# Kernel optimization log

Measured on AMD Instinct MI355X. Metric: run time of the kernel, lower is better.

The kernel has to match this reference:

```python
import jax, jax.numpy as jnp
import numpy as np

H, C = 2, 32  # heads, out_channels per head
NEG_SLOPE = 0.2


def gatv2_layer(h, src, dst, ea, W, b, We, att, bias, N):
    # shared lin_l = lin_r (share_weights=True)
    z = (h @ W + b).reshape(N, H, C)                      # [N,H,C]
    e = (ea @ We).reshape(-1, H, C)                        # [E',H,C]
    s = jax.nn.leaky_relu(z[dst] + z[src] + e, NEG_SLOPE)  # [E',H,C]
    alpha = jnp.einsum('ehc,hc->eh', s, att)               # [E',H]
    # segment softmax over destination neighborhoods
    m = jax.ops.segment_max(alpha, dst, num_segments=N)
    m = jnp.where(jnp.isfinite(m), m, 0.0)
    ex = jnp.exp(alpha - m[dst])
    denom = jax.ops.segment_sum(ex, dst, num_segments=N)
    a = ex / (denom[dst] + 1e-16)                          # [E',H]
    msg = (z[src] * a[:, :, None]).reshape(-1, H * C)      # [E',H*C]
    out = jax.ops.segment_sum(msg, dst, num_segments=N) + bias
    return out                                             # [N,H*C]


def setup_inputs() -> dict:
    key = jax.random.key(0)
    ks = jax.random.split(key, 16)
    N, E = 50000, 800000
    inp = {
        'x': jax.random.normal(ks[0], (N, 2), jnp.float32),
        'edge_index': jax.random.randint(ks[1], (2, E), 0, N, jnp.int64 if jax.config.jax_enable_x64 else jnp.int32).astype(jnp.int32),
        'edge_attr': jax.random.uniform(ks[2], (E, 2), jnp.float32),
        'dest_index': 123,
        'W0': jax.random.normal(ks[3], (2, 64), jnp.float32) * 0.5,
        'b0': jnp.zeros((64,), jnp.float32),
        'We0': jax.random.normal(ks[4], (2, 64), jnp.float32) * 0.5,
        'att0': jax.random.normal(ks[5], (H, C), jnp.float32) * 0.5,
        'bias0': jnp.zeros((64,), jnp.float32),
        'W1': jax.random.normal(ks[6], (64, 64), jnp.float32) * 0.125,
        'b1': jnp.zeros((64,), jnp.float32),
        'We1': jax.random.normal(ks[7], (2, 64), jnp.float32) * 0.5,
        'att1': jax.random.normal(ks[8], (H, C), jnp.float32) * 0.5,
        'bias1': jnp.zeros((64,), jnp.float32),
        'Wm1': jax.random.normal(ks[9], (194, 32), jnp.float32) * 0.07,
        'bm1': jnp.zeros((32,), jnp.float32),
        'Wm2': jax.random.normal(ks[10], (32, 1), jnp.float32) * 0.17,
        'bm2': jnp.zeros((1,), jnp.float32),
    }
    return inp


def reference(x, edge_index, edge_attr, dest_index,
              W0, b0, We0, att0, bias0,
              W1, b1, We1, att1, bias1,
              Wm1, bm1, Wm2, bm2):
    N = x.shape[0]
    # add self loops (fill_value='mean' for edge_attr)
    loops = jnp.arange(N, dtype=edge_index.dtype)
    src = jnp.concatenate([edge_index[0], loops])
    dst = jnp.concatenate([edge_index[1], loops])
    ea_sl = jnp.concatenate(
        [edge_attr, jnp.broadcast_to(edge_attr.mean(axis=0), (N, edge_attr.shape[1]))], axis=0)

    h = x
    h = jax.nn.elu(gatv2_layer(h, src, dst, ea_sl, W0, b0, We0, att0, bias0, N))
    h = jax.nn.elu(gatv2_layer(h, src, dst, ea_sl, W1, b1, We1, att1, bias1, N))

    goal = h[dest_index]                                   # [64]
    src_emb = h[edge_index[0]]                             # [E,64]
    dst_emb = h[edge_index[1]]                             # [E,64]
    goal_rep = jnp.broadcast_to(goal, (edge_index.shape[1], goal.shape[0]))
    edge_in = jnp.concatenate([src_emb, dst_emb, goal_rep, edge_attr], axis=-1)  # [E,194]
    hmlp = jax.nn.relu(edge_in @ Wm1 + bm1)
    logits = (hmlp @ Wm2 + bm2).squeeze(-1)                # [E]
    return logits
```

## Files before the change

kernel.cpp:

```cpp
#include <hip/hip_runtime.h>
#include <hip/hip_bf16.h>
#include <hip/hip_fp16.h>
#include <math.h>


typedef __attribute__((ext_vector_type(8))) short short8;
typedef __attribute__((ext_vector_type(4))) float f32x4;

#define BSH 6
#define CAP 2048
#define CH 4096

template <int IMM>
__device__ __forceinline__ float swz(float x) {
    return __int_as_float(__builtin_amdgcn_ds_swizzle(__float_as_int(x), IMM));
}

template <int CTRL>
__device__ __forceinline__ float dpp_add(float p) {
    int t = __builtin_amdgcn_update_dpp(0, __float_as_int(p), CTRL, 0xF, 0xF, true);
    return p + __int_as_float(t);
}

__device__ __forceinline__ short2 bsplit(float x) {
    unsigned u = __float_as_uint(x);
    short hi = (short)(u >> 16);
    float hif = __uint_as_float(u & 0xFFFF0000u);
    short lo = (short)(__float_as_uint(x - hif) >> 16);
    return make_short2(hi, lo);
}

__global__ __launch_bounds__(512) void setup_kernel(const float* __restrict__ W1,
                                                    const float* __restrict__ Wm1,
                                                    short* __restrict__ BfW1,
                                                    short* __restrict__ BfWm,
                                                    int* __restrict__ bucket_cursor,
                                                    float* __restrict__ easum, int nbuck) {
    if (blockIdx.x == 2) {
        for (int i = threadIdx.x; i < nbuck; i += 512) bucket_cursor[i] = i * CAP;
        if (threadIdx.x < 2) easum[threadIdx.x] = 0.f;
        return;
    }
    int snt = threadIdx.x >> 6;
    int lane = threadIdx.x & 63;
    int s = snt >> 2, nt = snt & 3;
    int col = nt * 16 + (lane & 15);
    short* Bf = blockIdx.x == 0 ? BfW1 : BfWm;
#pragma unroll
    for (int j = 0; j < 8; ++j) {
        int k = s * 32 + (lane >> 4) * 8 + j;
        float v;
        if (blockIdx.x == 0) {
            v = W1[k * 64 + col];
        } else {
            v = (col < 32) ? Wm1[k * 32 + col] : Wm1[(64 + k) * 32 + (col - 32)];
        }
        short2 t = bsplit(v);
        Bf[(snt * 2 + 0) * 512 + lane * 8 + j] = t.x;
        Bf[(snt * 2 + 1) * 512 + lane * 8 + j] = t.y;
    }
}

__global__ __launch_bounds__(256) void phaseA_kernel(const int* __restrict__ ei,
                                                     const float2* __restrict__ ea,
                                                     int* __restrict__ bucket_cursor,
                                                     float* __restrict__ easum,
                                                     float4* __restrict__ staged,
                                                     int E, int nbuck) {
    extern __shared__ int sm[];
    int* lcnt = sm;
    int* lbase = sm + nbuck;
    __shared__ float r0[4], r1[4];
    int tid = threadIdx.x;
    for (int i = tid; i < nbuck; i += 256) lcnt[i] = 0;
    __syncthreads();
    int base = blockIdx.x * CH;
    int end = min(base + CH, E);
    for (int i = base + tid; i < end; i += 256) {
        int d = ei[E + i];
        atomicAdd(&lcnt[d >> BSH], 1);
    }
    __syncthreads();
    for (int i = tid; i < nbuck; i += 256) {
        int c = lcnt[i];
        lbase[i] = c ? atomicAdd(&bucket_cursor[i], c) : 0;
        lcnt[i] = 0;
    }
    __syncthreads();
    float s0 = 0.f, s1 = 0.f;
    for (int i = base + tid; i < end; i += 256) {
        int s = ei[i], d = ei[E + i];
        float2 v = ea[i];
        s0 += v.x; s1 += v.y;
        int b = d >> BSH;
        int pos = lbase[b] + atomicAdd(&lcnt[b], 1);
        staged[pos] = make_float4(__int_as_float(s), v.x, v.y, __int_as_float(d));
    }
#pragma unroll
    for (int o = 32; o >= 1; o >>= 1) {
        s0 += __shfl_xor(s0, o);
        s1 += __shfl_xor(s1, o);
    }
    int wave = tid >> 6;
    if ((tid & 63) == 0) { r0[wave] = s0; r1[wave] = s1; }
    __syncthreads();
    if (tid == 0) {
        atomicAdd(&easum[0], r0[0] + r0[1] + r0[2] + r0[3]);
        atomicAdd(&easum[1], r1[0] + r1[1] + r1[2] + r1[3]);
    }
}

__global__ __launch_bounds__(512) void phaseB_mega(
    const float4* __restrict__ staged, const int* __restrict__ bucket_cursor,
    const float* __restrict__ easum, const float2* __restrict__ x,
    const float* __restrict__ W0, const float* __restrict__ b0,
    const float* __restrict__ We, const float* __restrict__ att,
    const float* __restrict__ bias, const short* __restrict__ Bf,
    const float* __restrict__ b1,
    int* __restrict__ row_ptr, float4* __restrict__ recs,
    __half* __restrict__ z16, int N, int E, int nbuck) {
    __shared__ int cnt64[64];
    __shared__ int offs[64];
    __shared__ int psum[512];
    __shared__ float acc6[64][6];
    __shared__ float h0s[64 * 64];
    int b = blockIdx.x;
    int n0g = b << BSH;
    int tid = threadIdx.x;
    int local = 0;
    for (int j = tid; j < b; j += 512) local += bucket_cursor[j] - j * CAP;
    psum[tid] = local;
    if (tid < 64) cnt64[tid] = 0;
    for (int i = tid; i < 64 * 6; i += 512) ((float*)acc6)[i] = 0.f;
    __syncthreads();
    for (int st = 256; st > 0; st >>= 1) {
        if (tid < st) psum[tid] += psum[tid + st];
        __syncthreads();
    }
    int bbase = psum[0] + 64 * b;
    int sbeg = b * CAP;
    int send = bucket_cursor[b];
    for (int i = sbeg + tid; i < send; i += 512) {
        int d = __float_as_int(staged[i].w);
        atomicAdd(&cnt64[d - n0g], 1);
    }
    __syncthreads();
    int node = n0g + tid;
    int tot = 0;
    if (tid < 64) {
        tot = cnt64[tid] + ((node < N) ? 1 : 0);
        offs[tid] = tot;
    }
    __syncthreads();
    for (int st = 1; st < 64; st <<= 1) {
        int v = 0;
        if (tid < 64) {
            v = offs[tid];
            if (tid >= st) v += offs[tid - st];
        }
        __syncthreads();
        if (tid < 64) offs[tid] = v;
        __syncthreads();
    }
    float invE = 1.f / (float)E;
    float m0 = easum[0] * invE, m1 = easum[1] * invE;
    if (tid < 64 && node < N) {
        int excl = bbase + offs[tid] - tot;
        row_ptr[node] = excl;
        recs[excl] = make_float4(__int_as_float(node), m0, m1, __int_as_float(node));
        offs[tid] = excl + 1;
    }
    int nodes_here = min(64, N - n0g);
    int nrec = (send - sbeg) + nodes_here;
    if (b == nbuck - 1 && tid == 0) row_ptr[N] = bbase + nrec;
    __syncthreads();
    for (int i = sbeg + tid; i < send; i += 512) {
        float4 r = staged[i];
        int d = __float_as_int(r.w);
        int pos = atomicAdd(&offs[d - n0g], 1);
        recs[pos] = r;
    }
    __syncthreads();

    int lane = tid & 63;
    int m = lane & 15, quad = lane >> 4;
    int wave = tid >> 6;
    {
        int c0 = quad * 8, c1 = 32 + c0;
        float w0a[8], w1a[8], ata[8], w0b[8], w1b[8], atb[8];
        float Wxa[8], Wya[8], bca[8], Wxb[8], Wyb[8], bcb[8];
#pragma unroll
        for (int j = 0; j < 8; ++j) {
            w0a[j] = We[c0 + j];  w1a[j] = We[64 + c0 + j];  ata[j] = att[c0 + j];
            w0b[j] = We[c1 + j];  w1b[j] = We[64 + c1 + j];  atb[j] = att[c1 + j];
            Wxa[j] = W0[c0 + j];  Wya[j] = W0[64 + c0 + j];  bca[j] = b0[c0 + j];
            Wxb[j] = W0[c1 + j];  Wyb[j] = W0[64 + c1 + j];  bcb[j] = b0[c1 + j];
        }
        int ntile = (nrec + 15) >> 4;
        for (int t = wave; t < ntile; t += 8) {
            int el = m * ntile + t;
            bool valid = el < nrec;
            int e = bbase + (valid ? el : nrec - 1);
            float4 r = recs[e];
            int s = __float_as_int(r.x);
            int d = __float_as_int(r.w);
            float2 xs = x[s];
            float2 xd = x[d];
            float P0 = 0.f, P1 = 0.f;
#pragma unroll
            for (int j = 0; j < 8; ++j) {
                float zs = fmaf(xs.x, Wxa[j], fmaf(xs.y, Wya[j], bca[j]));
                float zd = fmaf(xd.x, Wxa[j], fmaf(xd.y, Wya[j], bca[j]));
                float t0 = zd + zs + fmaf(r.y, w0a[j], r.z * w1a[j]);
                t0 = fmaxf(t0, 0.2f * t0);
                P0 = fmaf(t0, ata[j], P0);
                float zs1 = fmaf(xs.x, Wxb[j], fmaf(xs.y, Wyb[j], bcb[j]));
                float zd1 = fmaf(xd.x, Wxb[j], fmaf(xd.y, Wyb[j], bcb[j]));
                float t1 = zd1 + zs1 + fmaf(r.y, w0b[j], r.z * w1b[j]);
                t1 = fmaxf(t1, 0.2f * t1);
                P1 = fmaf(t1, atb[j], P1);
            }
            P0 += swz<0x401F>(P0);
            P1 += swz<0x401F>(P1);
            P0 += __shfl_xor(P0, 32);
            P1 += __shfl_xor(P1, 32);
            float w0 = __expf(fminf(P0, 60.f));
            float w1 = __expf(fminf(P1, 60.f));
            if (lane < 16 && valid) {
                int dl = d - n0g;
                atomicAdd(&acc6[dl][0], w0);
                atomicAdd(&acc6[dl][1], w0 * xs.x);
                atomicAdd(&acc6[dl][2], w0 * xs.y);
                atomicAdd(&acc6[dl][3], w1);
                atomicAdd(&acc6[dl][4], w1 * xs.x);
                atomicAdd(&acc6[dl][5], w1 * xs.y);
            }
        }
    }
    __syncthreads();

    for (int idx = tid; idx < nodes_here * 64; idx += 512) {
        int q = idx >> 6;
        int ch = idx & 63;
        int hsel = (ch >= 32) ? 3 : 0;
        float l  = acc6[q][hsel];
        float Sx = acc6[q][hsel + 1];
        float Sy = acc6[q][hsel + 2];
        float num = fmaf(W0[ch], Sx, fmaf(W0[64 + ch], Sy, b0[ch] * l));
        float v = num / (l + 1e-16f) + bias[ch];
        v = (v > 0.f) ? v : expm1f(v);
        h0s[idx] = v;
    }
    for (int idx = nodes_here * 64 + tid; idx < 64 * 64; idx += 512) h0s[idx] = 0.f;
    __syncthreads();

    int rowb = (wave & 3) * 16 + m;
    int ntb = (wave >> 2) * 2;
    f32x4 acc[2] = {{0.f, 0.f, 0.f, 0.f}, {0.f, 0.f, 0.f, 0.f}};
#pragma unroll
    for (int s = 0; s < 2; ++s) {
        const float* ap = h0s + rowb * 64 + s * 32 + quad * 8;
        float4 a0 = *(const float4*)ap;
        float4 a1 = *(const float4*)(ap + 4);
        short8 ahi, alo;
        short2 t;
        t = bsplit(a0.x); ahi[0] = t.x; alo[0] = t.y;
        t = bsplit(a0.y); ahi[1] = t.x; alo[1] = t.y;
        t = bsplit(a0.z); ahi[2] = t.x; alo[2] = t.y;
        t = bsplit(a0.w); ahi[3] = t.x; alo[3] = t.y;
        t = bsplit(a1.x); ahi[4] = t.x; alo[4] = t.y;
        t = bsplit(a1.y); ahi[5] = t.x; alo[5] = t.y;
        t = bsplit(a1.z); ahi[6] = t.x; alo[6] = t.y;
        t = bsplit(a1.w); ahi[7] = t.x; alo[7] = t.y;
#pragma unroll
        for (int u = 0; u < 2; ++u) {
            const short* bp = Bf + ((s * 4 + ntb + u) * 2) * 512 + lane * 8;
            short8 bhi = *(const short8*)bp;
            short8 blo = *(const short8*)(bp + 512);
            acc[u] = __builtin_amdgcn_mfma_f32_16x16x32_bf16(ahi, bhi, acc[u], 0, 0, 0);
            acc[u] = __builtin_amdgcn_mfma_f32_16x16x32_bf16(ahi, blo, acc[u], 0, 0, 0);
            acc[u] = __builtin_amdgcn_mfma_f32_16x16x32_bf16(alo, bhi, acc[u], 0, 0, 0);
        }
    }
#pragma unroll
    for (int u = 0; u < 2; ++u) {
        int col = (ntb + u) * 16 + m;
        float bj = b1[col];
#pragma unroll
        for (int r = 0; r < 4; ++r) {
            int orow = n0g + (wave & 3) * 16 + quad * 4 + r;
            if (orow < N) z16[(size_t)orow * 64 + col] = __float2half(acc[u][r] + bj);
        }
    }
}

__global__ __launch_bounds__(256) void agg1_kernel(
    const __half* __restrict__ z, const int* __restrict__ row_ptr,
    const float4* __restrict__ recs,
    const float* __restrict__ We, const float* __restrict__ att,
    const float* __restrict__ bias, float* __restrict__ hout, int N) {
    int gtid = blockIdx.x * blockDim.x + threadIdx.x;
    int n = gtid >> 6;
    if (n >= N) return;
    n = __builtin_amdgcn_readfirstlane(n);
    int lane = threadIdx.x & 63;
    int half = lane >> 5;
    int c = (lane & 31) * 2;

    float We0a = We[c],      We0b = We[c + 1];
    float We1a = We[64 + c], We1b = We[64 + c + 1];
    float atta = att[c],     attb = att[c + 1];
    float2 znf = __half22float2(*(const __half2*)(z + (size_t)n * 64 + c));

    int beg = row_ptr[n], end = row_ptr[n + 1];
    float ll[4] = {0.f, 0.f, 0.f, 0.f};
    float a0[4] = {0.f, 0.f, 0.f, 0.f};
    float a1[4] = {0.f, 0.f, 0.f, 0.f};
    for (int i = beg; i < end; i += 8) {
        float w[4]; float2 zs[4];
#pragma unroll
        for (int k = 0; k < 4; ++k) {
            int idx = i + 2 * k + half;
            int idc = idx < end ? idx : end - 1;
            float4 r = recs[idc];
            int s = __float_as_int(r.x);
            zs[k] = __half22float2(*(const __half2*)(z + (size_t)s * 64 + c));
            float sj0 = znf.x + zs[k].x + fmaf(r.y, We0a, r.z * We1a);
            float sj1 = znf.y + zs[k].y + fmaf(r.y, We0b, r.z * We1b);
            sj0 = fmaxf(sj0, 0.2f * sj0);
            sj1 = fmaxf(sj1, 0.2f * sj1);
            float p = fmaf(sj0, atta, sj1 * attb);
            p = dpp_add<0xB1>(p);
            p = dpp_add<0x4E>(p);
            p = dpp_add<0x141>(p);
            p = dpp_add<0x140>(p);
            float ww = __expf(fminf(p, 60.f));
            w[k] = (idx < end) ? ww : 0.f;
        }
#pragma unroll
        for (int k = 0; k < 4; ++k) {
            ll[k] += w[k];
            a0[k] = fmaf(w[k], zs[k].x, a0[k]);
            a1[k] = fmaf(w[k], zs[k].y, a1[k]);
        }
    }
    float l  = (ll[0] + ll[1]) + (ll[2] + ll[3]);
    float s0 = (a0[0] + a0[1]) + (a0[2] + a0[3]);
    float s1 = (a1[0] + a1[1]) + (a1[2] + a1[3]);
    l  += __shfl_xor(l, 32);
    s0 += __shfl_xor(s0, 32);
    s1 += __shfl_xor(s1, 32);
    float inv = 1.f / (l + 1e-16f);
    float v0 = s0 * inv + bias[c];
    float v1 = s1 * inv + bias[c + 1];
    v0 = (v0 > 0.f) ? v0 : expm1f(v0);
    v1 = (v1 > 0.f) ? v1 : expm1f(v1);
    *(float2*)(hout + (size_t)n * 64 + c) = make_float2(v0, v1);
}

__global__ __launch_bounds__(256) void mfma_gemm64(const float* __restrict__ h,
                                                   const short* __restrict__ Bf,
                                                   __half* __restrict__ out, int N,
                                                   const float* __restrict__ Wm1,
                                                   const float* __restrict__ bm1,
                                                   const int* __restrict__ dest,
                                                   float* __restrict__ gv) {
    int wave = threadIdx.x >> 6;
    int lane = threadIdx.x & 63;
    int n0 = blockIdx.x * 64 + wave * 16;
    if (n0 < N) {
        int m = lane & 15, quad = lane >> 4;
        int arow = n0 + m;
        if (arow > N - 1) arow = N - 1;
        f32x4 acc[4] = {{0.f, 0.f, 0.f, 0.f}, {0.f, 0.f, 0.f, 0.f},
                        {0.f, 0.f, 0.f, 0.f}, {0.f, 0.f, 0.f, 0.f}};
#pragma unroll
        for (int s = 0; s < 2; ++s) {
            const float* ap = h + (size_t)arow * 64 + s * 32 + quad * 8;
            float4 a0 = *(const float4*)ap;
            float4 a1 = *(const float4*)(ap + 4);
            short8 ahi, alo;
            short2 t;
            t = bsplit(a0.x); ahi[0] = t.x; alo[0] = t.y;
            t = bsplit(a0.y); ahi[1] = t.x; alo[1] = t.y;
            t = bsplit(a0.z); ahi[2] = t.x; alo[2] = t.y;
            t = bsplit(a0.w); ahi[3] = t.x; alo[3] = t.y;
            t = bsplit(a1.x); ahi[4] = t.x; alo[4] = t.y;
            t = bsplit(a1.y); ahi[5] = t.x; alo[5] = t.y;
            t = bsplit(a1.z); ahi[6] = t.x; alo[6] = t.y;
            t = bsplit(a1.w); ahi[7] = t.x; alo[7] = t.y;
#pragma unroll
            for (int nt = 0; nt < 4; ++nt) {
                const short* bp = Bf + ((s * 4 + nt) * 2) * 512 + lane * 8;
                short8 bhi = *(const short8*)bp;
                short8 blo = *(const short8*)(bp + 512);
                acc[nt] = __builtin_amdgcn_mfma_f32_16x16x32_bf16(ahi, bhi, acc[nt], 0, 0, 0);
                acc[nt] = __builtin_amdgcn_mfma_f32_16x16x32_bf16(ahi, blo, acc[nt], 0, 0, 0);
                acc[nt] = __builtin_amdgcn_mfma_f32_16x16x32_bf16(alo, bhi, acc[nt], 0, 0, 0);
            }
        }
#pragma unroll
        for (int nt = 0; nt < 4; ++nt) {
            int col = nt * 16 + m;
#pragma unroll
            for (int r = 0; r < 4; ++r) {
                int orow = n0 + quad * 4 + r;
                if (orow < N) out[(size_t)orow * 64 + col] = __float2half(acc[nt][r]);
            }
        }
    }
    if (gv && blockIdx.x == 0 && threadIdx.x < 32) {
        int dd = dest[0];
        int q = threadIdx.x;
        float acc2 = bm1[q];
        for (int k = 0; k < 64; ++k)
            acc2 = fmaf(h[(size_t)dd * 64 + k], Wm1[(128 + k) * 32 + q], acc2);
        gv[q] = acc2;
    }
}

__global__ __launch_bounds__(256) void edge_mlp_kernel(
    const int* __restrict__ ei, const float2* __restrict__ ea,
    const __half* __restrict__ hsd, const float* __restrict__ gvec,
    const float* __restrict__ WrowA, const float* __restrict__ WrowB,
    const float* __restrict__ Wm2, const float* __restrict__ bm2,
    float* __restrict__ out, int E) {
    int tid = blockIdx.x * blockDim.x + threadIdx.x;
    int e = tid >> 3;
    int j = tid & 7;
    if (e >= E) return;
    int s = ei[e], d = ei[E + e];
    float2 eav = ea[e];
    const __half2* ps = (const __half2*)(hsd + (size_t)s * 64 + j * 4);
    const __half2* pd = (const __half2*)(hsd + (size_t)d * 64 + 32 + j * 4);
    float2 a01 = __half22float2(ps[0]), a23 = __half22float2(ps[1]);
    float2 b01 = __half22float2(pd[0]), b23 = __half22float2(pd[1]);
    float4 g = *(const float4*)(gvec + j * 4);
    float4 wa = *(const float4*)(WrowA + j * 4);
    float4 wb = *(const float4*)(WrowB + j * 4);
    float4 w2 = *(const float4*)(Wm2 + j * 4);
    float acc = 0.f, v;
    v = fmaf(eav.x, wa.x, fmaf(eav.y, wb.x, a01.x + b01.x + g.x)); v = fmaxf(v, 0.f); acc = fmaf(v, w2.x, acc);
    v = fmaf(eav.x, wa.y, fmaf(eav.y, wb.y, a01.y + b01.y + g.y)); v = fmaxf(v, 0.f); acc = fmaf(v, w2.y, acc);
    v = fmaf(eav.x, wa.z, fmaf(eav.y, wb.z, a23.x + b23.x + g.z)); v = fmaxf(v, 0.f); acc = fmaf(v, w2.z, acc);
    v = fmaf(eav.x, wa.w, fmaf(eav.y, wb.w, a23.y + b23.y + g.w)); v = fmaxf(v, 0.f); acc = fmaf(v, w2.w, acc);
    acc = dpp_add<0xB1>(acc);
    acc = dpp_add<0x4E>(acc);
    acc = dpp_add<0x141>(acc);
    if (j == 0) out[e] = acc + bm2[0];
}

extern "C" void kernel_launch(void* const* d_in, const int* in_sizes, int n_in,
                              void* d_out, int out_size, void* d_ws, size_t ws_size,
                              hipStream_t stream) {
    const float* x     = (const float*)d_in[0];
    const int*   ei    = (const int*)d_in[1];
    const float* ea    = (const float*)d_in[2];
    const int*   dest  = (const int*)d_in[3];
    const float* W0    = (const float*)d_in[4];
    const float* b0    = (const float*)d_in[5];
    const float* We0   = (const float*)d_in[6];
    const float* att0  = (const float*)d_in[7];
    const float* bias0 = (const float*)d_in[8];
    const float* W1    = (const float*)d_in[9];
    const float* b1    = (const float*)d_in[10];
    const float* We1   = (const float*)d_in[11];
    const float* att1  = (const float*)d_in[12];
    const float* bias1 = (const float*)d_in[13];
    const float* Wm1   = (const float*)d_in[14];
    const float* bm1   = (const float*)d_in[15];
    const float* Wm2   = (const float*)d_in[16];
    const float* bm2   = (const float*)d_in[17];

    const int N = in_sizes[0] / 2;
    const int E = in_sizes[1] / 2;
    const int nbuck = (N + 63) >> BSH;
    const int nchunk = (E + CH - 1) / CH;

    char* ws = (char*)d_ws;
    size_t off = 0;
    auto alloc = [&](size_t bytes) -> void* {
        void* p = ws + off;
        off += bytes;
        off = (off + 255) & ~(size_t)255;
        return p;
    };
    int*    bucket_cursor = (int*)alloc((size_t)nbuck * 4);
    int*    row_ptr       = (int*)alloc((size_t)(N + 1) * 4);
    size_t  slack_bytes   = (size_t)nbuck * CAP * 16;
    float4* staged        = (float4*)alloc(slack_bytes);
    float4* recs          = (float4*)alloc((size_t)(E + N) * 16);
    __half* z16           = (__half*)alloc((size_t)N * 64 * 2);
    float*  hbuf          = (float*)alloc((size_t)N * 64 * 4);
    float*  easum         = (float*)alloc(8);
    float*  gvec          = (float*)alloc(32 * 4);
    short*  BfW1          = (short*)alloc(8192 * 2);
    short*  BfWm          = (short*)alloc(8192 * 2);
    __half* hsd16         = z16;

    dim3 blk(256);
    setup_kernel<<<3, 512, 0, stream>>>(W1, Wm1, BfW1, BfWm, bucket_cursor, easum, nbuck);
    phaseA_kernel<<<nchunk, blk, (size_t)nbuck * 8, stream>>>(ei, (const float2*)ea,
                                                              bucket_cursor, easum,
                                                              staged, E, nbuck);
    phaseB_mega<<<nbuck, 512, 0, stream>>>(staged, bucket_cursor, easum,
                                           (const float2*)x, W0, b0, We0, att0, bias0,
                                           BfW1, b1, row_ptr, recs, z16, N, E, nbuck);
    agg1_kernel<<<(N * 64 + 255) / 256, blk, 0, stream>>>(z16, row_ptr, recs,
                                                          We1, att1, bias1, hbuf, N);
    mfma_gemm64<<<(N + 63) / 64, blk, 0, stream>>>(hbuf, BfWm, hsd16, N,
                                                   Wm1, bm1, dest, gvec);
    edge_mlp_kernel<<<((size_t)E * 8 + 255) / 256, blk, 0, stream>>>(
        ei, (const float2*)ea, hsd16, gvec,
        Wm1 + 192 * 32, Wm1 + 193 * 32, Wm2, bm2, (float*)d_out, E);
}
```

Measured before the change: 256.9 us.

## Fuse layer-2 aggregation with MLP projection GEMM and shrink phaseB blocks

Merges the per-node layer-2 attention aggregation and the following MFMA projection GEMM into one kernel. Each 256-thread block aggregates 64 nodes into LDS and multiplies them by the packed MLP weights there, so the fp32 hidden buffer no longer makes a round trip through global memory and one launch is removed. The goal-vector dot product now reads from LDS in whichever block owns the dest node. phaseB_mega also drops from 512 to 256 threads, so each wave now covers all four output tiles of its 16 rows. The trade-off is fewer waves per block for latency hiding, and a serial 16-node loop per wave in the fused kernel.

```diff
diff --git a/kernel.cpp b/kernel.cpp
--- a/kernel.cpp
+++ b/kernel.cpp
@@ -110,7 +110,7 @@
     }
 }
 
-__global__ __launch_bounds__(512) void phaseB_mega(
+__global__ __launch_bounds__(256) void phaseB_mega(
     const float4* __restrict__ staged, const int* __restrict__ bucket_cursor,
     const float* __restrict__ easum, const float2* __restrict__ x,
     const float* __restrict__ W0, const float* __restrict__ b0,
@@ -121,26 +121,26 @@
     __half* __restrict__ z16, int N, int E, int nbuck) {
     __shared__ int cnt64[64];
     __shared__ int offs[64];
-    __shared__ int psum[512];
+    __shared__ int psum[256];
     __shared__ float acc6[64][6];
     __shared__ float h0s[64 * 64];
     int b = blockIdx.x;
     int n0g = b << BSH;
     int tid = threadIdx.x;
     int local = 0;
-    for (int j = tid; j < b; j += 512) local += bucket_cursor[j] - j * CAP;
+    for (int j = tid; j < b; j += 256) local += bucket_cursor[j] - j * CAP;
     psum[tid] = local;
     if (tid < 64) cnt64[tid] = 0;
-    for (int i = tid; i < 64 * 6; i += 512) ((float*)acc6)[i] = 0.f;
-    __syncthreads();
-    for (int st = 256; st > 0; st >>= 1) {
+    for (int i = tid; i < 64 * 6; i += 256) ((float*)acc6)[i] = 0.f;
+    __syncthreads();
+    for (int st = 128; st > 0; st >>= 1) {
         if (tid < st) psum[tid] += psum[tid + st];
         __syncthreads();
     }
     int bbase = psum[0] + 64 * b;
     int sbeg = b * CAP;
     int send = bucket_cursor[b];
-    for (int i = sbeg + tid; i < send; i += 512) {
+    for (int i = sbeg + tid; i < send; i += 256) {
         int d = __float_as_int(staged[i].w);
         atomicAdd(&cnt64[d - n0g], 1);
     }
@@ -174,7 +174,7 @@
     int nrec = (send - sbeg) + nodes_here;
     if (b == nbuck - 1 && tid == 0) row_ptr[N] = bbase + nrec;
     __syncthreads();
-    for (int i = sbeg + tid; i < send; i += 512) {
+    for (int i = sbeg + tid; i < send; i += 256) {
         float4 r = staged[i];
         int d = __float_as_int(r.w);
         int pos = atomicAdd(&offs[d - n0g], 1);
@@ -197,7 +197,7 @@
             Wxb[j] = W0[c1 + j];  Wyb[j] = W0[64 + c1 + j];  bcb[j] = b0[c1 + j];
         }
         int ntile = (nrec + 15) >> 4;
-        for (int t = wave; t < ntile; t += 8) {
+        for (int t = wave; t < ntile; t += 4) {
             int el = m * ntile + t;
             bool valid = el < nrec;
             int e = bbase + (valid ? el : nrec - 1);
@@ -239,7 +239,7 @@
     }
     __syncthreads();
 
-    for (int idx = tid; idx < nodes_here * 64; idx += 512) {
+    for (int idx = tid; idx < nodes_here * 64; idx += 256) {
         int q = idx >> 6;
         int ch = idx & 63;
         int hsel = (ch >= 32) ? 3 : 0;
@@ -251,12 +251,12 @@
         v = (v > 0.f) ? v : expm1f(v);
         h0s[idx] = v;
     }
-    for (int idx = nodes_here * 64 + tid; idx < 64 * 64; idx += 512) h0s[idx] = 0.f;
-    __syncthreads();
-
-    int rowb = (wave & 3) * 16 + m;
-    int ntb = (wave >> 2) * 2;
-    f32x4 acc[2] = {{0.f, 0.f, 0.f, 0.f}, {0.f, 0.f, 0.f, 0.f}};
+    for (int idx = nodes_here * 64 + tid; idx < 64 * 64; idx += 256) h0s[idx] = 0.f;
+    __syncthreads();
+
+    int rowb = wave * 16 + m;
+    f32x4 acc[4] = {{0.f, 0.f, 0.f, 0.f}, {0.f, 0.f, 0.f, 0.f},
+                    {0.f, 0.f, 0.f, 0.f}, {0.f, 0.f, 0.f, 0.f}};
 #pragma unroll
     for (int s = 0; s < 2; ++s) {
         const float* ap = h0s + rowb * 64 + s * 32 + quad * 8;
@@ -273,149 +273,152 @@
         t = bsplit(a1.z); ahi[6] = t.x; alo[6] = t.y;
         t = bsplit(a1.w); ahi[7] = t.x; alo[7] = t.y;
 #pragma unroll
-        for (int u = 0; u < 2; ++u) {
-            const short* bp = Bf + ((s * 4 + ntb + u) * 2) * 512 + lane * 8;
+        for (int nt = 0; nt < 4; ++nt) {
+            const short* bp = Bf + ((s * 4 + nt) * 2) * 512 + lane * 8;
             short8 bhi = *(const short8*)bp;
             short8 blo = *(const short8*)(bp + 512);
-            acc[u] = __builtin_amdgcn_mfma_f32_16x16x32_bf16(ahi, bhi, acc[u], 0, 0, 0);
-            acc[u] = __builtin_amdgcn_mfma_f32_16x16x32_bf16(ahi, blo, acc[u], 0, 0, 0);
-            acc[u] = __builtin_amdgcn_mfma_f32_16x16x32_bf16(alo, bhi, acc[u], 0, 0, 0);
-        }
-    }
-#pragma unroll
-    for (int u = 0; u < 2; ++u) {
-        int col = (ntb + u) * 16 + m;
+            acc[nt] = __builtin_amdgcn_mfma_f32_16x16x32_bf16(ahi, bhi, acc[nt], 0, 0, 0);
+            acc[nt] = __builtin_amdgcn_mfma_f32_16x16x32_bf16(ahi, blo, acc[nt], 0, 0, 0);
+            acc[nt] = __builtin_amdgcn_mfma_f32_16x16x32_bf16(alo, bhi, acc[nt], 0, 0, 0);
+        }
+    }
+#pragma unroll
+    for (int nt = 0; nt < 4; ++nt) {
+        int col = nt * 16 + m;
         float bj = b1[col];
 #pragma unroll
         for (int r = 0; r < 4; ++r) {
-            int orow = n0g + (wave & 3) * 16 + quad * 4 + r;
-            if (orow < N) z16[(size_t)orow * 64 + col] = __float2half(acc[u][r] + bj);
-        }
-    }
-}
-
-__global__ __launch_bounds__(256) void agg1_kernel(
+            int orow = n0g + wave * 16 + quad * 4 + r;
+            if (orow < N) z16[(size_t)orow * 64 + col] = __float2half(acc[nt][r] + bj);
+        }
+    }
+}
+
+__global__ __launch_bounds__(256) void agg1_gemm_kernel(
     const __half* __restrict__ z, const int* __restrict__ row_ptr,
     const float4* __restrict__ recs,
     const float* __restrict__ We, const float* __restrict__ att,
-    const float* __restrict__ bias, float* __restrict__ hout, int N) {
-    int gtid = blockIdx.x * blockDim.x + threadIdx.x;
-    int n = gtid >> 6;
-    if (n >= N) return;
-    n = __builtin_amdgcn_readfirstlane(n);
-    int lane = threadIdx.x & 63;
+    const float* __restrict__ bias, const short* __restrict__ Bf,
+    __half* __restrict__ out, int N,
+    const float* __restrict__ Wm1, const float* __restrict__ bm1,
+    const int* __restrict__ dest, float* __restrict__ gv) {
+    __shared__ float hlds[64 * 64];
+    int tid = threadIdx.x;
+    int wave = tid >> 6;
+    int lane = tid & 63;
     int half = lane >> 5;
     int c = (lane & 31) * 2;
+    int n0 = blockIdx.x * 64;
 
     float We0a = We[c],      We0b = We[c + 1];
     float We1a = We[64 + c], We1b = We[64 + c + 1];
     float atta = att[c],     attb = att[c + 1];
-    float2 znf = __half22float2(*(const __half2*)(z + (size_t)n * 64 + c));
-
-    int beg = row_ptr[n], end = row_ptr[n + 1];
-    float ll[4] = {0.f, 0.f, 0.f, 0.f};
-    float a0[4] = {0.f, 0.f, 0.f, 0.f};
-    float a1[4] = {0.f, 0.f, 0.f, 0.f};
-    for (int i = beg; i < end; i += 8) {
-        float w[4]; float2 zs[4];
-#pragma unroll
-        for (int k = 0; k < 4; ++k) {
-            int idx = i + 2 * k + half;
-            int idc = idx < end ? idx : end - 1;
-            float4 r = recs[idc];
-            int s = __float_as_int(r.x);
-            zs[k] = __half22float2(*(const __half2*)(z + (size_t)s * 64 + c));
-            float sj0 = znf.x + zs[k].x + fmaf(r.y, We0a, r.z * We1a);
-            float sj1 = znf.y + zs[k].y + fmaf(r.y, We0b, r.z * We1b);
-            sj0 = fmaxf(sj0, 0.2f * sj0);
-            sj1 = fmaxf(sj1, 0.2f * sj1);
-            float p = fmaf(sj0, atta, sj1 * attb);
-            p = dpp_add<0xB1>(p);
-            p = dpp_add<0x4E>(p);
-            p = dpp_add<0x141>(p);
-            p = dpp_add<0x140>(p);
-            float ww = __expf(fminf(p, 60.f));
-            w[k] = (idx < end) ? ww : 0.f;
-        }
-#pragma unroll
-        for (int k = 0; k < 4; ++k) {
-            ll[k] += w[k];
-            a0[k] = fmaf(w[k], zs[k].x, a0[k]);
-            a1[k] = fmaf(w[k], zs[k].y, a1[k]);
-        }
-    }
-    float l  = (ll[0] + ll[1]) + (ll[2] + ll[3]);
-    float s0 = (a0[0] + a0[1]) + (a0[2] + a0[3]);
-    float s1 = (a1[0] + a1[1]) + (a1[2] + a1[3]);
-    l  += __shfl_xor(l, 32);
-    s0 += __shfl_xor(s0, 32);
-    s1 += __shfl_xor(s1, 32);
-    float inv = 1.f / (l + 1e-16f);
-    float v0 = s0 * inv + bias[c];
-    float v1 = s1 * inv + bias[c + 1];
-    v0 = (v0 > 0.f) ? v0 : expm1f(v0);
-    v1 = (v1 > 0.f) ? v1 : expm1f(v1);
-    *(float2*)(hout + (size_t)n * 64 + c) = make_float2(v0, v1);
-}
-
-__global__ __launch_bounds__(256) void mfma_gemm64(const float* __restrict__ h,
-                                                   const short* __restrict__ Bf,
-                                                   __half* __restrict__ out, int N,
-                                                   const float* __restrict__ Wm1,
-                                                   const float* __restrict__ bm1,
-                                                   const int* __restrict__ dest,
-                                                   float* __restrict__ gv) {
-    int wave = threadIdx.x >> 6;
-    int lane = threadIdx.x & 63;
-    int n0 = blockIdx.x * 64 + wave * 16;
-    if (n0 < N) {
-        int m = lane & 15, quad = lane >> 4;
-        int arow = n0 + m;
-        if (arow > N - 1) arow = N - 1;
-        f32x4 acc[4] = {{0.f, 0.f, 0.f, 0.f}, {0.f, 0.f, 0.f, 0.f},
-                        {0.f, 0.f, 0.f, 0.f}, {0.f, 0.f, 0.f, 0.f}};
-#pragma unroll
-        for (int s = 0; s < 2; ++s) {
-            const float* ap = h + (size_t)arow * 64 + s * 32 + quad * 8;
-            float4 a0 = *(const float4*)ap;
-            float4 a1 = *(const float4*)(ap + 4);
-            short8 ahi, alo;
-            short2 t;
-            t = bsplit(a0.x); ahi[0] = t.x; alo[0] = t.y;
-            t = bsplit(a0.y); ahi[1] = t.x; alo[1] = t.y;
-            t = bsplit(a0.z); ahi[2] = t.x; alo[2] = t.y;
-            t = bsplit(a0.w); ahi[3] = t.x; alo[3] = t.y;
-            t = bsplit(a1.x); ahi[4] = t.x; alo[4] = t.y;
-            t = bsplit(a1.y); ahi[5] = t.x; alo[5] = t.y;
-            t = bsplit(a1.z); ahi[6] = t.x; alo[6] = t.y;
-            t = bsplit(a1.w); ahi[7] = t.x; alo[7] = t.y;
-#pragma unroll
-            for (int nt = 0; nt < 4; ++nt) {
-                const short* bp = Bf + ((s * 4 + nt) * 2) * 512 + lane * 8;
-                short8 bhi = *(const short8*)bp;
-                short8 blo = *(const short8*)(bp + 512);
-                acc[nt] = __builtin_amdgcn_mfma_f32_16x16x32_bf16(ahi, bhi, acc[nt], 0, 0, 0);
-                acc[nt] = __builtin_amdgcn_mfma_f32_16x16x32_bf16(ahi, blo, acc[nt], 0, 0, 0);
-                acc[nt] = __builtin_amdgcn_mfma_f32_16x16x32_bf16(alo, bhi, acc[nt], 0, 0, 0);
+    float bsa = bias[c],     bsb = bias[c + 1];
+
+    for (int t = 0; t < 16; ++t) {
+        int row = wave * 16 + t;
+        int n = n0 + row;
+        if (n < N) {
+            float2 znf = __half22float2(*(const __half2*)(z + (size_t)n * 64 + c));
+            int beg = row_ptr[n], end = row_ptr[n + 1];
+            float ll[4] = {0.f, 0.f, 0.f, 0.f};
+            float a0[4] = {0.f, 0.f, 0.f, 0.f};
+            float a1[4] = {0.f, 0.f, 0.f, 0.f};
+            for (int i = beg; i < end; i += 8) {
+                float w[4]; float2 zs[4];
+#pragma unroll
+                for (int k = 0; k < 4; ++k) {
+                    int idx = i + 2 * k + half;
+                    int idc = idx < end ? idx : end - 1;
+                    float4 r = recs[idc];
+                    int s = __float_as_int(r.x);
+                    zs[k] = __half22float2(*(const __half2*)(z + (size_t)s * 64 + c));
+                    float sj0 = znf.x + zs[k].x + fmaf(r.y, We0a, r.z * We1a);
+                    float sj1 = znf.y + zs[k].y + fmaf(r.y, We0b, r.z * We1b);
+                    sj0 = fmaxf(sj0, 0.2f * sj0);
+                    sj1 = fmaxf(sj1, 0.2f * sj1);
+                    float p = fmaf(sj0, atta, sj1 * attb);
+                    p = dpp_add<0xB1>(p);
+                    p = dpp_add<0x4E>(p);
+                    p = dpp_add<0x141>(p);
+                    p = dpp_add<0x140>(p);
+                    float ww = __expf(fminf(p, 60.f));
+                    w[k] = (idx < end) ? ww : 0.f;
+                }
+#pragma unroll
+                for (int k = 0; k < 4; ++k) {
+                    ll[k] += w[k];
+                    a0[k] = fmaf(w[k], zs[k].x, a0[k]);
+                    a1[k] = fmaf(w[k], zs[k].y, a1[k]);
+                }
             }
-        }
+            float l  = (ll[0] + ll[1]) + (ll[2] + ll[3]);
+            float s0 = (a0[0] + a0[1]) + (a0[2] + a0[3]);
+            float s1 = (a1[0] + a1[1]) + (a1[2] + a1[3]);
+            l  += __shfl_xor(l, 32);
+            s0 += __shfl_xor(s0, 32);
+            s1 += __shfl_xor(s1, 32);
+            float inv = 1.f / (l + 1e-16f);
+            float v0 = s0 * inv + bsa;
+            float v1 = s1 * inv + bsb;
+            v0 = (v0 > 0.f) ? v0 : expm1f(v0);
+            v1 = (v1 > 0.f) ? v1 : expm1f(v1);
+            if (half == 0)
+                *(float2*)(hlds + row * 64 + c) = make_float2(v0, v1);
+        } else if (half == 0) {
+            *(float2*)(hlds + row * 64 + c) = make_float2(0.f, 0.f);
+        }
+    }
+    __syncthreads();
+
+    int m = lane & 15, quad = lane >> 4;
+    int rowb = wave * 16 + m;
+    f32x4 acc[4] = {{0.f, 0.f, 0.f, 0.f}, {0.f, 0.f, 0.f, 0.f},
+                    {0.f, 0.f, 0.f, 0.f}, {0.f, 0.f, 0.f, 0.f}};
+#pragma unroll
+    for (int s = 0; s < 2; ++s) {
+        const float* ap = hlds + rowb * 64 + s * 32 + quad * 8;
+        float4 a0 = *(const float4*)ap;
+        float4 a1 = *(const float4*)(ap + 4);
+        short8 ahi, alo;
+        short2 t;
+        t = bsplit(a0.x); ahi[0] = t.x; alo[0] = t.y;
+        t = bsplit(a0.y); ahi[1] = t.x; alo[1] = t.y;
+        t = bsplit(a0.z); ahi[2] = t.x; alo[2] = t.y;
+        t = bsplit(a0.w); ahi[3] = t.x; alo[3] = t.y;
+        t = bsplit(a1.x); ahi[4] = t.x; alo[4] = t.y;
+        t = bsplit(a1.y); ahi[5] = t.x; alo[5] = t.y;
+        t = bsplit(a1.z); ahi[6] = t.x; alo[6] = t.y;
+        t = bsplit(a1.w); ahi[7] = t.x; alo[7] = t.y;
 #pragma unroll
         for (int nt = 0; nt < 4; ++nt) {
-            int col = nt * 16 + m;
-#pragma unroll
-            for (int r = 0; r < 4; ++r) {
-                int orow = n0 + quad * 4 + r;
-                if (orow < N) out[(size_t)orow * 64 + col] = __float2half(acc[nt][r]);
-            }
-        }
-    }
-    if (gv && blockIdx.x == 0 && threadIdx.x < 32) {
+            const short* bp = Bf + ((s * 4 + nt) * 2) * 512 + lane * 8;
+            short8 bhi = *(const short8*)bp;
+            short8 blo = *(const short8*)(bp + 512);
+            acc[nt] = __builtin_amdgcn_mfma_f32_16x16x32_bf16(ahi, bhi, acc[nt], 0, 0, 0);
+            acc[nt] = __builtin_amdgcn_mfma_f32_16x16x32_bf16(ahi, blo, acc[nt], 0, 0, 0);
+            acc[nt] = __builtin_amdgcn_mfma_f32_16x16x32_bf16(alo, bhi, acc[nt], 0, 0, 0);
+        }
+    }
+#pragma unroll
+    for (int nt = 0; nt < 4; ++nt) {
+        int col = nt * 16 + m;
+#pragma unroll
+        for (int r = 0; r < 4; ++r) {
+            int orow = n0 + wave * 16 + quad * 4 + r;
+            if (orow < N) out[(size_t)orow * 64 + col] = __float2half(acc[nt][r]);
+        }
+    }
+    if (tid < 32) {
         int dd = dest[0];
-        int q = threadIdx.x;
-        float acc2 = bm1[q];
-        for (int k = 0; k < 64; ++k)
-            acc2 = fmaf(h[(size_t)dd * 64 + k], Wm1[(128 + k) * 32 + q], acc2);
-        gv[q] = acc2;
+        if ((dd >> 6) == (int)blockIdx.x) {
+            int q = tid;
+            const float* hr = hlds + (dd & 63) * 64;
+            float acc2 = bm1[q];
+            for (int k = 0; k < 64; ++k)
+                acc2 = fmaf(hr[k], Wm1[(128 + k) * 32 + q], acc2);
+            gv[q] = acc2;
+        }
     }
 }
 
@@ -491,25 +494,23 @@
     float4* staged        = (float4*)alloc(slack_bytes);
     float4* recs          = (float4*)alloc((size_t)(E + N) * 16);
     __half* z16           = (__half*)alloc((size_t)N * 64 * 2);
-    float*  hbuf          = (float*)alloc((size_t)N * 64 * 4);
+    __half* hsd16         = (__half*)alloc((size_t)N * 64 * 2);
     float*  easum         = (float*)alloc(8);
     float*  gvec          = (float*)alloc(32 * 4);
     short*  BfW1          = (short*)alloc(8192 * 2);
     short*  BfWm          = (short*)alloc(8192 * 2);
-    __half* hsd16         = z16;
 
     dim3 blk(256);
     setup_kernel<<<3, 512, 0, stream>>>(W1, Wm1, BfW1, BfWm, bucket_cursor, easum, nbuck);
     phaseA_kernel<<<nchunk, blk, (size_t)nbuck * 8, stream>>>(ei, (const float2*)ea,
                                                               bucket_cursor, easum,
                                                               staged, E, nbuck);
-    phaseB_mega<<<nbuck, 512, 0, stream>>>(staged, bucket_cursor, easum,
+    phaseB_mega<<<nbuck, blk, 0, stream>>>(staged, bucket_cursor, easum,
                                            (const float2*)x, W0, b0, We0, att0, bias0,
                                            BfW1, b1, row_ptr, recs, z16, N, E, nbuck);
-    agg1_kernel<<<(N * 64 + 255) / 256, blk, 0, stream>>>(z16, row_ptr, recs,
-                                                          We1, att1, bias1, hbuf, N);
-    mfma_gemm64<<<(N + 63) / 64, blk, 0, stream>>>(hbuf, BfWm, hsd16, N,
-                                                   Wm1, bm1, dest, gvec);
+    agg1_gemm_kernel<<<nbuck, blk, 0, stream>>>(z16, row_ptr, recs,
+                                                We1, att1, bias1, BfWm,
+                                                hsd16, N, Wm1, bm1, dest, gvec);
     edge_mlp_kernel<<<((size_t)E * 8 + 255) / 256, blk, 0, stream>>>(
         ei, (const float2*)ea, hsd16, gvec,
         Wm1 + 192 * 32, Wm1 + 193 * 32, Wm2, bm2, (float*)d_out, E);
```

Result: slower. 281.4 us (+9.5%).

## Use wave-shuffle scans and software-prefetch edge records in phaseB_mega

Applied to the files above, without the earlier changes.

Replaces the shared-memory tree reduction and Hillis-Steele scan with wave-level shuffle reductions and scans, removing many __syncthreads barriers. The layer-0 attention loop now prefetches the next tile's record and its x gathers while computing the current tile, so memory latency overlaps with compute. Adds launch_bounds(512,2) to request two blocks per CU, which may cap registers and cause spills given the extra live prefetch state.

```diff
diff --git a/kernel.cpp b/kernel.cpp
--- a/kernel.cpp
+++ b/kernel.cpp
@@ -110,7 +110,7 @@
     }
 }
 
-__global__ __launch_bounds__(512) void phaseB_mega(
+__global__ __launch_bounds__(512, 2) void phaseB_mega(
     const float4* __restrict__ staged, const int* __restrict__ bucket_cursor,
     const float* __restrict__ easum, const float2* __restrict__ x,
     const float* __restrict__ W0, const float* __restrict__ b0,
@@ -121,23 +121,24 @@
     __half* __restrict__ z16, int N, int E, int nbuck) {
     __shared__ int cnt64[64];
     __shared__ int offs[64];
-    __shared__ int psum[512];
+    __shared__ int psum8[8];
     __shared__ float acc6[64][6];
     __shared__ float h0s[64 * 64];
     int b = blockIdx.x;
     int n0g = b << BSH;
     int tid = threadIdx.x;
+    int lane = tid & 63;
+    int wave = tid >> 6;
     int local = 0;
     for (int j = tid; j < b; j += 512) local += bucket_cursor[j] - j * CAP;
-    psum[tid] = local;
+#pragma unroll
+    for (int o = 32; o >= 1; o >>= 1) local += __shfl_xor(local, o);
     if (tid < 64) cnt64[tid] = 0;
     for (int i = tid; i < 64 * 6; i += 512) ((float*)acc6)[i] = 0.f;
-    __syncthreads();
-    for (int st = 256; st > 0; st >>= 1) {
-        if (tid < st) psum[tid] += psum[tid + st];
-        __syncthreads();
-    }
-    int bbase = psum[0] + 64 * b;
+    if (lane == 0) psum8[wave] = local;
+    __syncthreads();
+    int bbase = 64 * b + psum8[0] + psum8[1] + psum8[2] + psum8[3]
+                       + psum8[4] + psum8[5] + psum8[6] + psum8[7];
     int sbeg = b * CAP;
     int send = bucket_cursor[b];
     for (int i = sbeg + tid; i < send; i += 512) {
@@ -145,34 +146,27 @@
         atomicAdd(&cnt64[d - n0g], 1);
     }
     __syncthreads();
-    int node = n0g + tid;
-    int tot = 0;
-    if (tid < 64) {
-        tot = cnt64[tid] + ((node < N) ? 1 : 0);
-        offs[tid] = tot;
-    }
-    __syncthreads();
-    for (int st = 1; st < 64; st <<= 1) {
-        int v = 0;
-        if (tid < 64) {
-            v = offs[tid];
-            if (tid >= st) v += offs[tid - st];
-        }
-        __syncthreads();
-        if (tid < 64) offs[tid] = v;
-        __syncthreads();
-    }
+    int nodes_here = min(64, N - n0g);
+    int nrec = (send - sbeg) + nodes_here;
     float invE = 1.f / (float)E;
     float m0 = easum[0] * invE, m1 = easum[1] * invE;
-    if (tid < 64 && node < N) {
-        int excl = bbase + offs[tid] - tot;
-        row_ptr[node] = excl;
-        recs[excl] = make_float4(__int_as_float(node), m0, m1, __int_as_float(node));
-        offs[tid] = excl + 1;
-    }
-    int nodes_here = min(64, N - n0g);
-    int nrec = (send - sbeg) + nodes_here;
-    if (b == nbuck - 1 && tid == 0) row_ptr[N] = bbase + nrec;
+    if (wave == 0) {
+        int node = n0g + lane;
+        int tot = cnt64[lane] + ((node < N) ? 1 : 0);
+        int v = tot;
+#pragma unroll
+        for (int st = 1; st < 64; st <<= 1) {
+            int u = __shfl_up(v, st);
+            if (lane >= st) v += u;
+        }
+        if (node < N) {
+            int excl = bbase + v - tot;
+            row_ptr[node] = excl;
+            recs[excl] = make_float4(__int_as_float(node), m0, m1, __int_as_float(node));
+            offs[lane] = excl + 1;
+        }
+        if (b == nbuck - 1 && lane == 0) row_ptr[N] = bbase + nrec;
+    }
     __syncthreads();
     for (int i = sbeg + tid; i < send; i += 512) {
         float4 r = staged[i];
@@ -182,9 +176,7 @@
     }
     __syncthreads();
 
-    int lane = tid & 63;
     int m = lane & 15, quad = lane >> 4;
-    int wave = tid >> 6;
     {
         int c0 = quad * 8, c1 = 32 + c0;
         float w0a[8], w1a[8], ata[8], w0b[8], w1b[8], atb[8];
@@ -197,28 +189,45 @@
             Wxb[j] = W0[c1 + j];  Wyb[j] = W0[64 + c1 + j];  bcb[j] = b0[c1 + j];
         }
         int ntile = (nrec + 15) >> 4;
-        for (int t = wave; t < ntile; t += 8) {
+        float4 rA = make_float4(0.f, 0.f, 0.f, 0.f);
+        float2 xsA = make_float2(0.f, 0.f), xdA = make_float2(0.f, 0.f);
+        bool validA = false;
+        int t = wave;
+        if (t < ntile) {
             int el = m * ntile + t;
-            bool valid = el < nrec;
-            int e = bbase + (valid ? el : nrec - 1);
-            float4 r = recs[e];
-            int s = __float_as_int(r.x);
-            int d = __float_as_int(r.w);
-            float2 xs = x[s];
-            float2 xd = x[d];
+            validA = el < nrec;
+            rA = recs[bbase + (validA ? el : nrec - 1)];
+            xsA = x[__float_as_int(rA.x)];
+            xdA = x[__float_as_int(rA.w)];
+        }
+        while (t < ntile) {
+            int tn = t + 8;
+            bool haveB = tn < ntile;
+            bool validB = false;
+            float4 rB = make_float4(0.f, 0.f, 0.f, 0.f);
+            if (haveB) {
+                int el = m * ntile + tn;
+                validB = el < nrec;
+                rB = recs[bbase + (validB ? el : nrec - 1)];
+            }
             float P0 = 0.f, P1 = 0.f;
 #pragma unroll
             for (int j = 0; j < 8; ++j) {
-                float zs = fmaf(xs.x, Wxa[j], fmaf(xs.y, Wya[j], bca[j]));
-                float zd = fmaf(xd.x, Wxa[j], fmaf(xd.y, Wya[j], bca[j]));
-                float t0 = zd + zs + fmaf(r.y, w0a[j], r.z * w1a[j]);
+                float zs = fmaf(xsA.x, Wxa[j], fmaf(xsA.y, Wya[j], bca[j]));
+                float zd = fmaf(xdA.x, Wxa[j], fmaf(xdA.y, Wya[j], bca[j]));
+                float t0 = zd + zs + fmaf(rA.y, w0a[j], rA.z * w1a[j]);
                 t0 = fmaxf(t0, 0.2f * t0);
                 P0 = fmaf(t0, ata[j], P0);
-                float zs1 = fmaf(xs.x, Wxb[j], fmaf(xs.y, Wyb[j], bcb[j]));
-                float zd1 = fmaf(xd.x, Wxb[j], fmaf(xd.y, Wyb[j], bcb[j]));
-                float t1 = zd1 + zs1 + fmaf(r.y, w0b[j], r.z * w1b[j]);
+                float zs1 = fmaf(xsA.x, Wxb[j], fmaf(xsA.y, Wyb[j], bcb[j]));
+                float zd1 = fmaf(xdA.x, Wxb[j], fmaf(xdA.y, Wyb[j], bcb[j]));
+                float t1 = zd1 + zs1 + fmaf(rA.y, w0b[j], rA.z * w1b[j]);
                 t1 = fmaxf(t1, 0.2f * t1);
                 P1 = fmaf(t1, atb[j], P1);
+            }
+            float2 xsB = make_float2(0.f, 0.f), xdB = make_float2(0.f, 0.f);
+            if (haveB) {
+                xsB = x[__float_as_int(rB.x)];
+                xdB = x[__float_as_int(rB.w)];
             }
             P0 += swz<0x401F>(P0);
             P1 += swz<0x401F>(P1);
@@ -226,15 +235,17 @@
             P1 += __shfl_xor(P1, 32);
             float w0 = __expf(fminf(P0, 60.f));
             float w1 = __expf(fminf(P1, 60.f));
-            if (lane < 16 && valid) {
-                int dl = d - n0g;
+            if (lane < 16 && validA) {
+                int dl = __float_as_int(rA.w) - n0g;
                 atomicAdd(&acc6[dl][0], w0);
-                atomicAdd(&acc6[dl][1], w0 * xs.x);
-                atomicAdd(&acc6[dl][2], w0 * xs.y);
+                atomicAdd(&acc6[dl][1], w0 * xsA.x);
+                atomicAdd(&acc6[dl][2], w0 * xsA.y);
                 atomicAdd(&acc6[dl][3], w1);
-                atomicAdd(&acc6[dl][4], w1 * xs.x);
-                atomicAdd(&acc6[dl][5], w1 * xs.y);
+                atomicAdd(&acc6[dl][4], w1 * xsA.x);
+                atomicAdd(&acc6[dl][5], w1 * xsA.y);
             }
+            rA = rB; xsA = xsB; xdA = xdB; validA = validB;
+            t = tn;
         }
     }
     __syncthreads();
```

Result: slower. 271.8 us (+5.8%).

## Restructure phaseB to read staged edges directly and overlap CSR scatter with MFMA

Applied to the files above, without the earlier changes.

The layer-0 attention pass now reads edges straight from the staged bucket instead of first building the CSR records. Degree counts are gathered inside that pass, and self-loop weights are computed analytically per node. The prefix sums use wave shuffles instead of multi-barrier shared-memory reductions. The CSR record scatter is moved to waves 4-7 so it runs concurrently with the layer-1 MFMA matmul on waves 0-3, which now each cover all four column tiles. This removes several barriers and an extra pass over staged data, at the cost of load imbalance between the wave groups.

```diff
diff --git a/kernel.cpp b/kernel.cpp
--- a/kernel.cpp
+++ b/kernel.cpp
@@ -121,70 +121,33 @@
     __half* __restrict__ z16, int N, int E, int nbuck) {
     __shared__ int cnt64[64];
     __shared__ int offs[64];
-    __shared__ int psum[512];
+    __shared__ int psum8[8];
     __shared__ float acc6[64][6];
     __shared__ float h0s[64 * 64];
     int b = blockIdx.x;
     int n0g = b << BSH;
     int tid = threadIdx.x;
+    int lane = tid & 63;
+    int wave = tid >> 6;
     int local = 0;
     for (int j = tid; j < b; j += 512) local += bucket_cursor[j] - j * CAP;
-    psum[tid] = local;
+#pragma unroll
+    for (int o = 32; o >= 1; o >>= 1) local += __shfl_xor(local, o);
     if (tid < 64) cnt64[tid] = 0;
     for (int i = tid; i < 64 * 6; i += 512) ((float*)acc6)[i] = 0.f;
-    __syncthreads();
-    for (int st = 256; st > 0; st >>= 1) {
-        if (tid < st) psum[tid] += psum[tid + st];
-        __syncthreads();
-    }
-    int bbase = psum[0] + 64 * b;
+    if (lane == 0) psum8[wave] = local;
+    __syncthreads();
+    int bbase = 64 * b + psum8[0] + psum8[1] + psum8[2] + psum8[3]
+                       + psum8[4] + psum8[5] + psum8[6] + psum8[7];
     int sbeg = b * CAP;
     int send = bucket_cursor[b];
-    for (int i = sbeg + tid; i < send; i += 512) {
-        int d = __float_as_int(staged[i].w);
-        atomicAdd(&cnt64[d - n0g], 1);
-    }
-    __syncthreads();
-    int node = n0g + tid;
-    int tot = 0;
-    if (tid < 64) {
-        tot = cnt64[tid] + ((node < N) ? 1 : 0);
-        offs[tid] = tot;
-    }
-    __syncthreads();
-    for (int st = 1; st < 64; st <<= 1) {
-        int v = 0;
-        if (tid < 64) {
-            v = offs[tid];
-            if (tid >= st) v += offs[tid - st];
-        }
-        __syncthreads();
-        if (tid < 64) offs[tid] = v;
-        __syncthreads();
-    }
+    int nsl = send - sbeg;
+    int nodes_here = min(64, N - n0g);
+    int nrec = nsl + nodes_here;
     float invE = 1.f / (float)E;
     float m0 = easum[0] * invE, m1 = easum[1] * invE;
-    if (tid < 64 && node < N) {
-        int excl = bbase + offs[tid] - tot;
-        row_ptr[node] = excl;
-        recs[excl] = make_float4(__int_as_float(node), m0, m1, __int_as_float(node));
-        offs[tid] = excl + 1;
-    }
-    int nodes_here = min(64, N - n0g);
-    int nrec = (send - sbeg) + nodes_here;
-    if (b == nbuck - 1 && tid == 0) row_ptr[N] = bbase + nrec;
-    __syncthreads();
-    for (int i = sbeg + tid; i < send; i += 512) {
-        float4 r = staged[i];
-        int d = __float_as_int(r.w);
-        int pos = atomicAdd(&offs[d - n0g], 1);
-        recs[pos] = r;
-    }
-    __syncthreads();
-
-    int lane = tid & 63;
+
     int m = lane & 15, quad = lane >> 4;
-    int wave = tid >> 6;
     {
         int c0 = quad * 8, c1 = 32 + c0;
         float w0a[8], w1a[8], ata[8], w0b[8], w1b[8], atb[8];
@@ -196,12 +159,11 @@
             Wxa[j] = W0[c0 + j];  Wya[j] = W0[64 + c0 + j];  bca[j] = b0[c0 + j];
             Wxb[j] = W0[c1 + j];  Wyb[j] = W0[64 + c1 + j];  bcb[j] = b0[c1 + j];
         }
-        int ntile = (nrec + 15) >> 4;
-        for (int t = wave; t < ntile; t += 8) {
-            int el = m * ntile + t;
-            bool valid = el < nrec;
-            int e = bbase + (valid ? el : nrec - 1);
-            float4 r = recs[e];
+        int npass = (nsl + 15) >> 4;
+        for (int p = wave; p < npass; p += 8) {
+            int idx = p * 16 + m;
+            bool valid = idx < nsl;
+            float4 r = staged[sbeg + (valid ? idx : nsl - 1)];
             int s = __float_as_int(r.x);
             int d = __float_as_int(r.w);
             float2 xs = x[s];
@@ -234,62 +196,101 @@
                 atomicAdd(&acc6[dl][3], w1);
                 atomicAdd(&acc6[dl][4], w1 * xs.x);
                 atomicAdd(&acc6[dl][5], w1 * xs.y);
+                atomicAdd(&cnt64[dl], 1);
             }
         }
     }
     __syncthreads();
 
-    for (int idx = tid; idx < nodes_here * 64; idx += 512) {
-        int q = idx >> 6;
-        int ch = idx & 63;
-        int hsel = (ch >= 32) ? 3 : 0;
-        float l  = acc6[q][hsel];
-        float Sx = acc6[q][hsel + 1];
-        float Sy = acc6[q][hsel + 2];
-        float num = fmaf(W0[ch], Sx, fmaf(W0[64 + ch], Sy, b0[ch] * l));
-        float v = num / (l + 1e-16f) + bias[ch];
-        v = (v > 0.f) ? v : expm1f(v);
-        h0s[idx] = v;
-    }
-    for (int idx = nodes_here * 64 + tid; idx < 64 * 64; idx += 512) h0s[idx] = 0.f;
-    __syncthreads();
-
-    int rowb = (wave & 3) * 16 + m;
-    int ntb = (wave >> 2) * 2;
-    f32x4 acc[2] = {{0.f, 0.f, 0.f, 0.f}, {0.f, 0.f, 0.f, 0.f}};
-#pragma unroll
-    for (int s = 0; s < 2; ++s) {
-        const float* ap = h0s + rowb * 64 + s * 32 + quad * 8;
-        float4 a0 = *(const float4*)ap;
-        float4 a1 = *(const float4*)(ap + 4);
-        short8 ahi, alo;
-        short2 t;
-        t = bsplit(a0.x); ahi[0] = t.x; alo[0] = t.y;
-        t = bsplit(a0.y); ahi[1] = t.x; alo[1] = t.y;
-        t = bsplit(a0.z); ahi[2] = t.x; alo[2] = t.y;
-        t = bsplit(a0.w); ahi[3] = t.x; alo[3] = t.y;
-        t = bsplit(a1.x); ahi[4] = t.x; alo[4] = t.y;
-        t = bsplit(a1.y); ahi[5] = t.x; alo[5] = t.y;
-        t = bsplit(a1.z); ahi[6] = t.x; alo[6] = t.y;
-        t = bsplit(a1.w); ahi[7] = t.x; alo[7] = t.y;
-#pragma unroll
-        for (int u = 0; u < 2; ++u) {
-            const short* bp = Bf + ((s * 4 + ntb + u) * 2) * 512 + lane * 8;
-            short8 bhi = *(const short8*)bp;
-            short8 blo = *(const short8*)(bp + 512);
-            acc[u] = __builtin_amdgcn_mfma_f32_16x16x32_bf16(ahi, bhi, acc[u], 0, 0, 0);
-            acc[u] = __builtin_amdgcn_mfma_f32_16x16x32_bf16(ahi, blo, acc[u], 0, 0, 0);
-            acc[u] = __builtin_amdgcn_mfma_f32_16x16x32_bf16(alo, bhi, acc[u], 0, 0, 0);
-        }
-    }
-#pragma unroll
-    for (int u = 0; u < 2; ++u) {
-        int col = (ntb + u) * 16 + m;
-        float bj = b1[col];
-#pragma unroll
-        for (int r = 0; r < 4; ++r) {
-            int orow = n0g + (wave & 3) * 16 + quad * 4 + r;
-            if (orow < N) z16[(size_t)orow * 64 + col] = __float2half(acc[u][r] + bj);
+    if (wave == 0) {
+        int node = n0g + lane;
+        int tot = cnt64[lane] + ((node < N) ? 1 : 0);
+        int v = tot;
+#pragma unroll
+        for (int st = 1; st < 64; st <<= 1) {
+            int u = __shfl_up(v, st);
+            if (lane >= st) v += u;
+        }
+        if (node < N) {
+            int excl = bbase + v - tot;
+            row_ptr[node] = excl;
+            recs[excl] = make_float4(__int_as_float(node), m0, m1, __int_as_float(node));
+            offs[lane] = excl + 1;
+        }
+        if (b == nbuck - 1 && lane == 0) row_ptr[N] = bbase + nrec;
+    }
+    for (int k = 0; k < 8; ++k) {
+        int q = wave + 8 * k;
+        int ch = lane;
+        int node = n0g + q;
+        float hv = 0.f;
+        if (node < N) {
+            float2 xn = x[node];
+            float W0c = W0[ch], W0c2 = W0[64 + ch], b0c = b0[ch];
+            float zn = fmaf(xn.x, W0c, fmaf(xn.y, W0c2, b0c));
+            float ts = fmaf(2.f, zn, fmaf(m0, We[ch], m1 * We[64 + ch]));
+            ts = fmaxf(ts, 0.2f * ts);
+            float p = ts * att[ch];
+#pragma unroll
+            for (int o = 1; o <= 16; o <<= 1) p += __shfl_xor(p, o);
+            float wself = __expf(fminf(p, 60.f));
+            int hsel = (ch >= 32) ? 3 : 0;
+            float l  = acc6[q][hsel]     + wself;
+            float Sx = acc6[q][hsel + 1] + wself * xn.x;
+            float Sy = acc6[q][hsel + 2] + wself * xn.y;
+            float num = fmaf(W0c, Sx, fmaf(W0c2, Sy, b0c * l));
+            float v = num / (l + 1e-16f) + bias[ch];
+            hv = (v > 0.f) ? v : expm1f(v);
+        }
+        h0s[q * 64 + ch] = hv;
+    }
+    __syncthreads();
+
+    if (wave < 4) {
+        int rowb = wave * 16 + m;
+        f32x4 acc[4] = {{0.f, 0.f, 0.f, 0.f}, {0.f, 0.f, 0.f, 0.f},
+                        {0.f, 0.f, 0.f, 0.f}, {0.f, 0.f, 0.f, 0.f}};
+#pragma unroll
+        for (int s = 0; s < 2; ++s) {
+            const float* ap = h0s + rowb * 64 + s * 32 + quad * 8;
+            float4 a0 = *(const float4*)ap;
+            float4 a1 = *(const float4*)(ap + 4);
+            short8 ahi, alo;
+            short2 t;
+            t = bsplit(a0.x); ahi[0] = t.x; alo[0] = t.y;
+            t = bsplit(a0.y); ahi[1] = t.x; alo[1] = t.y;
+            t = bsplit(a0.z); ahi[2] = t.x; alo[2] = t.y;
+            t = bsplit(a0.w); ahi[3] = t.x; alo[3] = t.y;
+            t = bsplit(a1.x); ahi[4] = t.x; alo[4] = t.y;
+            t = bsplit(a1.y); ahi[5] = t.x; alo[5] = t.y;
+            t = bsplit(a1.z); ahi[6] = t.x; alo[6] = t.y;
+            t = bsplit(a1.w); ahi[7] = t.x; alo[7] = t.y;
+#pragma unroll
+            for (int nt = 0; nt < 4; ++nt) {
+                const short* bp = Bf + ((s * 4 + nt) * 2) * 512 + lane * 8;
+                short8 bhi = *(const short8*)bp;
+                short8 blo = *(const short8*)(bp + 512);
+                acc[nt] = __builtin_amdgcn_mfma_f32_16x16x32_bf16(ahi, bhi, acc[nt], 0, 0, 0);
+                acc[nt] = __builtin_amdgcn_mfma_f32_16x16x32_bf16(ahi, blo, acc[nt], 0, 0, 0);
+                acc[nt] = __builtin_amdgcn_mfma_f32_16x16x32_bf16(alo, bhi, acc[nt], 0, 0, 0);
+            }
+        }
+#pragma unroll
+        for (int nt = 0; nt < 4; ++nt) {
+            int col = nt * 16 + m;
+            float bj = b1[col];
+#pragma unroll
+            for (int r = 0; r < 4; ++r) {
+                int orow = n0g + wave * 16 + quad * 4 + r;
+                if (orow < N) z16[(size_t)orow * 64 + col] = __float2half(acc[nt][r] + bj);
+            }
+        }
+    } else {
+        for (int i = sbeg + (tid - 256); i < send; i += 256) {
+            float4 r = staged[i];
+            int d = __float_as_int(r.w);
+            int pos = atomicAdd(&offs[d - n0g], 1);
+            recs[pos] = r;
         }
     }
 }
```

After: 272.1 us. 1.06x slower.
